# Optimization experiments

Measured on AMD Instinct MI355X. Metric: run time of the kernel, lower is better.

The kernel has to match this reference:

```python
import jax, jax.numpy as jnp
import numpy as np

NUM_CLASSES = 4
SIGMA_S = 1.0
SIGMA_Z = 1.0


def _rbf_gram(x, sigma):
    # x: [N, d] -> [N, N] Gaussian kernel exp(-||xi-xj||^2 / (2 sigma^2))
    sq = jnp.sum(x * x, axis=-1)
    d2 = sq[:, None] + sq[None, :] - 2.0 * (x @ x.T)
    d2 = jnp.maximum(d2, 0.0)
    return jnp.exp(-d2 / (2.0 * sigma * sigma))


def _double_center(K):
    # Faithful to: K = mean_center(K, dim=0); K_m = mean_center(K.t(), dim=0)
    K = K - jnp.mean(K, axis=0, keepdims=True)
    K = K.T
    K = K - jnp.mean(K, axis=0, keepdims=True)
    return K


def setup_inputs() -> dict:
    key = jax.random.key(0)
    kz, ks = jax.random.split(key)
    z = jax.random.normal(kz, (8192, 128), dtype=jnp.float32)
    s = jax.random.randint(ks, (8192,), 0, NUM_CLASSES, dtype=jnp.int64)
    norm = jnp.float32(1.0)
    return {"z": z, "s": s, "norm": norm}


def reference(z, s, norm):
    n = z.shape[0]
    s_onehot = jax.nn.one_hot(s, NUM_CLASSES, dtype=z.dtype)  # format_onehot
    K_sm = _double_center(_rbf_gram(s_onehot, SIGMA_S))
    K_zm = _double_center(_rbf_gram(z, SIGMA_Z))
    # trace(K_zm.T @ K_sm) == sum(K_zm * K_sm): O(N^2) instead of O(N^3)
    dep = jnp.sum(K_zm * K_sm)
    dep = dep / (norm * (n * n))
    return dep
```

## Files before the change

### kernel.cpp

```cpp
#include <hip/hip_runtime.h>
#include <hip/hip_bf16.h>

typedef float f32x4 __attribute__((ext_vector_type(4)));

#define ZD      128
#define BT      128
#define D2_CUT  60.0f
#define D2_TRIG 70.0f

__device__ __forceinline__ void async_copy16(const unsigned char* g,
                                             unsigned char* l) {
    __builtin_amdgcn_global_load_lds(
        (const __attribute__((address_space(1))) unsigned int*)g,
        (__attribute__((address_space(3))) unsigned int*)l,
        16, 0, 0);
}

__global__ __launch_bounds__(256) void dep_prep(
    const float* __restrict__ z, const int* __restrict__ s,
    float* __restrict__ sq, float* __restrict__ sqmin,
    unsigned char* __restrict__ zb8, float* __restrict__ pvals,
    const float* __restrict__ norm, float* __restrict__ out, int N)
{
    __shared__ float part[32][33];
    const int tid  = threadIdx.x;
    const int wave = tid >> 6, lane = tid & 63;
    const int half = lane >> 5, c = lane & 31;
    const int r0   = blockIdx.x * 32;

    if (blockIdx.x == 0 && wave == 2) {
        int c0 = 0, c1 = 0, c2 = 0, c3 = 0;
        for (int it = lane; it < N / 4; it += 64) {
            int4 v = ((const int4*)s)[it];
            c0 += (v.x == 0) + (v.y == 0) + (v.z == 0) + (v.w == 0);
            c1 += (v.x == 1) + (v.y == 1) + (v.z == 1) + (v.w == 1);
            c2 += (v.x == 2) + (v.y == 2) + (v.z == 2) + (v.w == 2);
            c3 += (v.x == 3) + (v.y == 3) + (v.z == 3) + (v.w == 3);
        }
        #pragma unroll
        for (int off = 1; off < 64; off <<= 1) {
            c0 += __shfl_xor(c0, off, 64);
            c1 += __shfl_xor(c1, off, 64);
            c2 += __shfl_xor(c2, off, 64);
            c3 += __shfl_xor(c3, off, 64);
        }
        if (lane == 0) {
            const double n = (double)N;
            const double p0 = c0 / n, p1 = c1 / n, p2 = c2 / n, p3 = c3 / n;
            const double sump2 = p0*p0 + p1*p1 + p2*p2 + p3*p3;
            const double scale = (1.0 - exp(-1.0)) / ((double)norm[0] * n * n);
            pvals[0] = (float)p0; pvals[1] = (float)p1;
            pvals[2] = (float)p2; pvals[3] = (float)p3;
            pvals[4] = (float)sump2;
            pvals[5] = (float)scale;
            const double c2sum = (double)c0*c0 + (double)c1*c1
                               + (double)c2*c2 + (double)c3*c3;
            const double diag = n - c2sum / n;
            out[0] = (float)(diag * scale);
        }
    }

    #pragma unroll
    for (int i = 0; i < 4; ++i) {
        const int rloc = wave * 8 + i * 2 + half;
        const int r    = r0 + rloc;
        float4 v = ((const float4*)z)[r * 32 + c];
        int pk = __builtin_amdgcn_cvt_pk_fp8_f32(v.x, v.y, 0, false);
        pk     = __builtin_amdgcn_cvt_pk_fp8_f32(v.z, v.w, pk, true);
        ((unsigned int*)zb8)[r * 32 + c] = (unsigned int)pk;
        part[rloc][c] = v.x*v.x + v.y*v.y + v.z*v.z + v.w*v.w;
    }
    __syncthreads();

    if (wave == 0 && lane < 32) {
        float sum = 0.f;
        #pragma unroll
        for (int k = 0; k < 32; ++k) sum += part[lane][k];
        sq[r0 + lane] = sum;
        float mn = sum;
        #pragma unroll
        for (int off = 1; off < 32; off <<= 1)
            mn = fminf(mn, __shfl_xor(mn, off, 64));
        if (lane == 0) sqmin[blockIdx.x] = mn;
    }
}

__global__ __launch_bounds__(256, 4) void dep_pair(
    const unsigned char* __restrict__ zb8, const float* __restrict__ sq,
    const float* __restrict__ sqmin, const int* __restrict__ s,
    const float* __restrict__ pvals, float* __restrict__ out, int T)
{
    __shared__ unsigned char Apan[BT * ZD];
    __shared__ unsigned char Bpan[BT * ZD];

    const int tid  = threadIdx.x;
    const int wave = tid >> 6, lane = tid & 63;

    const int t = blockIdx.x;
    #define TRI_BASE(x) ((x) * T - ((x) * ((x) - 1)) / 2)
    double disc = (2.0 * T + 1.0) * (2.0 * T + 1.0) - 8.0 * (double)t;
    int ti = (int)((2.0 * T + 1.0 - sqrt(disc)) * 0.5);
    if (ti < 0) ti = 0;
    if (ti > T - 1) ti = T - 1;
    while (ti + 1 < T && TRI_BASE(ti + 1) <= t) ++ti;
    while (ti > 0 && TRI_BASE(ti) > t) --ti;
    const int tj = ti + (t - TRI_BASE(ti));
    #undef TRI_BASE

    const int i0 = ti * BT, j0 = tj * BT;
    const int wi = wave >> 1, wj = wave & 1;
    const int l15 = lane & 15, quad = lane >> 4;

    {
        const unsigned char* gAp = zb8 + (size_t)i0 * ZD;
        const unsigned char* gBp = zb8 + (size_t)j0 * ZD;
        const int rl  = lane >> 3;
        const int cch = lane & 7;
        const int gch = cch ^ rl;
        #pragma unroll
        for (int k = 0; k < 4; ++k) {
            const int r0i = (wave * 4 + k) * 8;
            const size_t go = (size_t)(r0i + rl) * ZD + (gch << 4);
            async_copy16(gAp + go, Apan + r0i * ZD);
            async_copy16(gBp + go, Bpan + r0i * ZD);
        }
    }
    __syncthreads();

    f32x4 accv[4][4];
    #pragma unroll
    for (int a = 0; a < 4; ++a)
        #pragma unroll
        for (int b = 0; b < 4; ++b)
            accv[a][b] = (f32x4){0.f, 0.f, 0.f, 0.f};

    const int sub = (quad & 1) * 8;
    #pragma unroll
    for (int kc = 0; kc < 4; ++kc) {
        long af[4], bfr[4];
        const int ch = (kc * 2 + (quad >> 1)) ^ (l15 & 7);
        #pragma unroll
        for (int it = 0; it < 4; ++it) {
            const int row = wi * 64 + it * 16 + l15;
            af[it] = *(const long*)(Apan + row * ZD + (ch << 4) + sub);
        }
        #pragma unroll
        for (int jt = 0; jt < 4; ++jt) {
            const int row = wj * 64 + jt * 16 + l15;
            bfr[jt] = *(const long*)(Bpan + row * ZD + (ch << 4) + sub);
        }
        #pragma unroll
        for (int it = 0; it < 4; ++it)
            #pragma unroll
            for (int jt = 0; jt < 4; ++jt)
                accv[it][jt] = __builtin_amdgcn_mfma_f32_16x16x32_fp8_fp8(
                    af[it], bfr[jt], accv[it][jt], 0, 0, 0);
    }

    float m = -1e30f;
    #pragma unroll
    for (int it = 0; it < 4; ++it)
        #pragma unroll
        for (int jt = 0; jt < 4; ++jt) {
            const f32x4 v = accv[it][jt];
            m = fmaxf(m, fmaxf(fmaxf(v[0], v[1]), fmaxf(v[2], v[3])));
        }
    #pragma unroll
    for (int off = 1; off < 64; off <<= 1)
        m = fmaxf(m, __shfl_xor(m, off, 64));

    const int gA = (i0 >> 5) + wi * 2;
    const int gB = (j0 >> 5) + wj * 2;
    const float sminA = fminf(sqmin[gA], sqmin[gA + 1]);
    const float sminB = fminf(sqmin[gB], sqmin[gB + 1]);
    const float bound = sminA + sminB - 2.0f * m;

    if (bound < D2_TRIG) {
        const float p0 = pvals[0], p1 = pvals[1],
                    p2 = pvals[2], p3 = pvals[3];
        const float sump2 = pvals[4], scale = pvals[5];
        const float p[4] = {p0, p1, p2, p3};

        const int ibase = i0 + wi * 64, jbase = j0 + wj * 64;
        float sqj[4];
        #pragma unroll
        for (int jt = 0; jt < 4; ++jt) sqj[jt] = sq[jbase + jt * 16 + l15];

        float local = 0.f;
        #pragma unroll
        for (int it = 0; it < 4; ++it) {
            #pragma unroll
            for (int r = 0; r < 4; ++r) {
                const int i = ibase + it * 16 + quad * 4 + r;
                const float sqi = sq[i];
                #pragma unroll
                for (int jt = 0; jt < 4; ++jt) {
                    const int j = jbase + jt * 16 + l15;
                    float d2 = sqi + sqj[jt] - 2.0f * accv[it][jt][r];
                    d2 = fmaxf(d2, 0.0f);
                    if (d2 < D2_CUT && i != j) {
                        const int si = s[i], sj = s[j];
                        const float w = (si == sj ? 1.0f : 0.0f)
                                      - p[si] - p[sj] + sump2;
                        local += w * __expf(-0.5f * d2);
                    }
                }
            }
        }
        if (ti < tj) local *= 2.0f;

        #pragma unroll
        for (int off = 32; off > 0; off >>= 1)
            local += __shfl_down(local, off, 64);
        if (lane == 0 && local != 0.0f)
            atomicAdd(out, local * scale);
    }
}

extern "C" void kernel_launch(void* const* d_in, const int* in_sizes, int n_in,
                              void* d_out, int out_size, void* d_ws, size_t ws_size,
                              hipStream_t stream)
{
    const float* z    = (const float*)d_in[0];
    const int*   s    = (const int*)d_in[1];
    const float* norm = (const float*)d_in[2];
    float* out = (float*)d_out;

    const int N = in_sizes[1];
    const int T = N / BT;

    char* ws = (char*)d_ws;
    float*         pvals = (float*)ws;
    float*         sq    = (float*)(ws + 64);
    float*         sqmin = (float*)(ws + 64 + (size_t)N * 4);
    unsigned char* zb8   = (unsigned char*)(ws + 64 + (size_t)N * 4
                                            + (size_t)(N / 32) * 4);

    dep_prep<<<N / 32, 256, 0, stream>>>(z, s, sq, sqmin, zb8, pvals,
                                         norm, out, N);
    const int nblocks = T * (T + 1) / 2;
    dep_pair<<<nblocks, 256, 0, stream>>>(zb8, sq, sqmin, s, pvals, out, T);
}
```

Baseline: 77.91 us.

## Make pair kernel persistent with double-buffered LDS prefetch and tile map

The pair kernel becomes a persistent grid of 512 blocks that loops over triangular tile pairs, prefetching the next tile's A/B panels into a second LDS buffer while the current tile is computed. The per-block sqrt-based triangular index decode is replaced by a lookup table that the prep kernel writes. The aim is to hide global-to-LDS load latency and cut launch and decode overhead. In exchange LDS use doubles and the occupancy hint drops to 2 blocks per CU, so there is less parallelism across waves.

```diff
diff --git a/kernel.cpp b/kernel.cpp
--- a/kernel.cpp
+++ b/kernel.cpp
@@ -20,13 +20,21 @@
     const float* __restrict__ z, const int* __restrict__ s,
     float* __restrict__ sq, float* __restrict__ sqmin,
     unsigned char* __restrict__ zb8, float* __restrict__ pvals,
-    const float* __restrict__ norm, float* __restrict__ out, int N)
+    int* __restrict__ tmap, const float* __restrict__ norm,
+    float* __restrict__ out, int N, int T)
 {
     __shared__ float part[32][33];
     const int tid  = threadIdx.x;
     const int wave = tid >> 6, lane = tid & 63;
     const int half = lane >> 5, c = lane & 31;
     const int r0   = blockIdx.x * 32;
+
+    if (blockIdx.x == 0 && wave == 1 && lane < T) {
+        const int ti   = lane;
+        const int base = ti * T - (ti * (ti - 1)) / 2;
+        for (int tj = ti; tj < T; ++tj)
+            tmap[base + (tj - ti)] = (ti << 8) | tj;
+    }
 
     if (blockIdx.x == 0 && wave == 2) {
         int c0 = 0, c1 = 0, c2 = 0, c3 = 0;
@@ -85,135 +93,150 @@
     }
 }
 
-__global__ __launch_bounds__(256, 4) void dep_pair(
+__global__ __launch_bounds__(256, 2) void dep_pair(
     const unsigned char* __restrict__ zb8, const float* __restrict__ sq,
     const float* __restrict__ sqmin, const int* __restrict__ s,
-    const float* __restrict__ pvals, float* __restrict__ out, int T)
+    const float* __restrict__ pvals, const int* __restrict__ tmap,
+    float* __restrict__ out, int NT)
 {
-    __shared__ unsigned char Apan[BT * ZD];
-    __shared__ unsigned char Bpan[BT * ZD];
+    __shared__ unsigned char pan[2][2][BT * ZD];
 
     const int tid  = threadIdx.x;
     const int wave = tid >> 6, lane = tid & 63;
-
-    const int t = blockIdx.x;
-    #define TRI_BASE(x) ((x) * T - ((x) * ((x) - 1)) / 2)
-    double disc = (2.0 * T + 1.0) * (2.0 * T + 1.0) - 8.0 * (double)t;
-    int ti = (int)((2.0 * T + 1.0 - sqrt(disc)) * 0.5);
-    if (ti < 0) ti = 0;
-    if (ti > T - 1) ti = T - 1;
-    while (ti + 1 < T && TRI_BASE(ti + 1) <= t) ++ti;
-    while (ti > 0 && TRI_BASE(ti) > t) --ti;
-    const int tj = ti + (t - TRI_BASE(ti));
-    #undef TRI_BASE
-
-    const int i0 = ti * BT, j0 = tj * BT;
-    const int wi = wave >> 1, wj = wave & 1;
-    const int l15 = lane & 15, quad = lane >> 4;
-
-    {
-        const unsigned char* gAp = zb8 + (size_t)i0 * ZD;
-        const unsigned char* gBp = zb8 + (size_t)j0 * ZD;
-        const int rl  = lane >> 3;
-        const int cch = lane & 7;
-        const int gch = cch ^ rl;
+    const int wi   = wave >> 1, wj = wave & 1;
+    const int l15  = lane & 15, quad = lane >> 4;
+    const int rl   = lane >> 3, cch = lane & 7;
+    const int gch  = cch ^ rl;
+
+    int t = blockIdx.x;
+    if (t >= NT) return;
+
+    int mt = tmap[t];
+    int ti = mt >> 8, tj = mt & 255;
+
+    auto stage = [&](int sti, int stj, int buf) {
+        const unsigned char* gA = zb8 + (size_t)sti * BT * ZD;
+        const unsigned char* gB = zb8 + (size_t)stj * BT * ZD;
         #pragma unroll
         for (int k = 0; k < 4; ++k) {
             const int r0i = (wave * 4 + k) * 8;
             const size_t go = (size_t)(r0i + rl) * ZD + (gch << 4);
-            async_copy16(gAp + go, Apan + r0i * ZD);
-            async_copy16(gBp + go, Bpan + r0i * ZD);
-        }
-    }
+            async_copy16(gA + go, &pan[buf][0][r0i * ZD]);
+            async_copy16(gB + go, &pan[buf][1][r0i * ZD]);
+        }
+    };
+
+    stage(ti, tj, 0);
     __syncthreads();
-
-    f32x4 accv[4][4];
-    #pragma unroll
-    for (int a = 0; a < 4; ++a)
-        #pragma unroll
-        for (int b = 0; b < 4; ++b)
-            accv[a][b] = (f32x4){0.f, 0.f, 0.f, 0.f};
-
-    const int sub = (quad & 1) * 8;
-    #pragma unroll
-    for (int kc = 0; kc < 4; ++kc) {
-        long af[4], bfr[4];
-        const int ch = (kc * 2 + (quad >> 1)) ^ (l15 & 7);
-        #pragma unroll
-        for (int it = 0; it < 4; ++it) {
-            const int row = wi * 64 + it * 16 + l15;
-            af[it] = *(const long*)(Apan + row * ZD + (ch << 4) + sub);
-        }
-        #pragma unroll
-        for (int jt = 0; jt < 4; ++jt) {
-            const int row = wj * 64 + jt * 16 + l15;
-            bfr[jt] = *(const long*)(Bpan + row * ZD + (ch << 4) + sub);
-        }
+    int p = 0;
+
+    while (true) {
+        const int tn = t + gridDim.x;
+        const bool have = (tn < NT);
+        int nti = 0, ntj = 0;
+        if (have) {
+            const int m2 = tmap[tn];
+            nti = m2 >> 8; ntj = m2 & 255;
+            stage(nti, ntj, p ^ 1);
+        }
+
+        const int i0 = ti * BT, j0 = tj * BT;
+        const unsigned char* Apan = &pan[p][0][0];
+        const unsigned char* Bpan = &pan[p][1][0];
+
+        f32x4 accv[4][4];
+        #pragma unroll
+        for (int a = 0; a < 4; ++a)
+            #pragma unroll
+            for (int b = 0; b < 4; ++b)
+                accv[a][b] = (f32x4){0.f, 0.f, 0.f, 0.f};
+
+        const int sub = (quad & 1) * 8;
+        #pragma unroll
+        for (int kc = 0; kc < 4; ++kc) {
+            long af[4], bfr[4];
+            const int ch = (kc * 2 + (quad >> 1)) ^ (l15 & 7);
+            #pragma unroll
+            for (int it = 0; it < 4; ++it) {
+                const int row = wi * 64 + it * 16 + l15;
+                af[it] = *(const long*)(Apan + row * ZD + (ch << 4) + sub);
+            }
+            #pragma unroll
+            for (int jt = 0; jt < 4; ++jt) {
+                const int row = wj * 64 + jt * 16 + l15;
+                bfr[jt] = *(const long*)(Bpan + row * ZD + (ch << 4) + sub);
+            }
+            #pragma unroll
+            for (int it = 0; it < 4; ++it)
+                #pragma unroll
+                for (int jt = 0; jt < 4; ++jt)
+                    accv[it][jt] = __builtin_amdgcn_mfma_f32_16x16x32_fp8_fp8(
+                        af[it], bfr[jt], accv[it][jt], 0, 0, 0);
+        }
+
+        float m = -1e30f;
         #pragma unroll
         for (int it = 0; it < 4; ++it)
             #pragma unroll
+            for (int jt = 0; jt < 4; ++jt) {
+                const f32x4 v = accv[it][jt];
+                m = fmaxf(m, fmaxf(fmaxf(v[0], v[1]), fmaxf(v[2], v[3])));
+            }
+        #pragma unroll
+        for (int off = 1; off < 64; off <<= 1)
+            m = fmaxf(m, __shfl_xor(m, off, 64));
+
+        const int gA = (i0 >> 5) + wi * 2;
+        const int gB = (j0 >> 5) + wj * 2;
+        const float sminA = fminf(sqmin[gA], sqmin[gA + 1]);
+        const float sminB = fminf(sqmin[gB], sqmin[gB + 1]);
+        const float bound = sminA + sminB - 2.0f * m;
+
+        if (bound < D2_TRIG) {
+            const float p0 = pvals[0], p1 = pvals[1],
+                        p2 = pvals[2], p3 = pvals[3];
+            const float sump2 = pvals[4], scale = pvals[5];
+            const float pr[4] = {p0, p1, p2, p3};
+
+            const int ibase = i0 + wi * 64, jbase = j0 + wj * 64;
+            float sqj[4];
+            #pragma unroll
             for (int jt = 0; jt < 4; ++jt)
-                accv[it][jt] = __builtin_amdgcn_mfma_f32_16x16x32_fp8_fp8(
-                    af[it], bfr[jt], accv[it][jt], 0, 0, 0);
-    }
-
-    float m = -1e30f;
-    #pragma unroll
-    for (int it = 0; it < 4; ++it)
-        #pragma unroll
-        for (int jt = 0; jt < 4; ++jt) {
-            const f32x4 v = accv[it][jt];
-            m = fmaxf(m, fmaxf(fmaxf(v[0], v[1]), fmaxf(v[2], v[3])));
-        }
-    #pragma unroll
-    for (int off = 1; off < 64; off <<= 1)
-        m = fmaxf(m, __shfl_xor(m, off, 64));
-
-    const int gA = (i0 >> 5) + wi * 2;
-    const int gB = (j0 >> 5) + wj * 2;
-    const float sminA = fminf(sqmin[gA], sqmin[gA + 1]);
-    const float sminB = fminf(sqmin[gB], sqmin[gB + 1]);
-    const float bound = sminA + sminB - 2.0f * m;
-
-    if (bound < D2_TRIG) {
-        const float p0 = pvals[0], p1 = pvals[1],
-                    p2 = pvals[2], p3 = pvals[3];
-        const float sump2 = pvals[4], scale = pvals[5];
-        const float p[4] = {p0, p1, p2, p3};
-
-        const int ibase = i0 + wi * 64, jbase = j0 + wj * 64;
-        float sqj[4];
-        #pragma unroll
-        for (int jt = 0; jt < 4; ++jt) sqj[jt] = sq[jbase + jt * 16 + l15];
-
-        float local = 0.f;
-        #pragma unroll
-        for (int it = 0; it < 4; ++it) {
-            #pragma unroll
-            for (int r = 0; r < 4; ++r) {
-                const int i = ibase + it * 16 + quad * 4 + r;
-                const float sqi = sq[i];
+                sqj[jt] = sq[jbase + jt * 16 + l15];
+
+            float local = 0.f;
+            #pragma unroll
+            for (int it = 0; it < 4; ++it) {
                 #pragma unroll
-                for (int jt = 0; jt < 4; ++jt) {
-                    const int j = jbase + jt * 16 + l15;
-                    float d2 = sqi + sqj[jt] - 2.0f * accv[it][jt][r];
-                    d2 = fmaxf(d2, 0.0f);
-                    if (d2 < D2_CUT && i != j) {
-                        const int si = s[i], sj = s[j];
-                        const float w = (si == sj ? 1.0f : 0.0f)
-                                      - p[si] - p[sj] + sump2;
-                        local += w * __expf(-0.5f * d2);
+                for (int r = 0; r < 4; ++r) {
+                    const int i = ibase + it * 16 + quad * 4 + r;
+                    const float sqi = sq[i];
+                    #pragma unroll
+                    for (int jt = 0; jt < 4; ++jt) {
+                        const int j = jbase + jt * 16 + l15;
+                        float d2 = sqi + sqj[jt] - 2.0f * accv[it][jt][r];
+                        d2 = fmaxf(d2, 0.0f);
+                        if (d2 < D2_CUT && i != j) {
+                            const int si = s[i], sj = s[j];
+                            const float w = (si == sj ? 1.0f : 0.0f)
+                                          - pr[si] - pr[sj] + sump2;
+                            local += w * __expf(-0.5f * d2);
+                        }
                     }
                 }
             }
-        }
-        if (ti < tj) local *= 2.0f;
-
-        #pragma unroll
-        for (int off = 32; off > 0; off >>= 1)
-            local += __shfl_down(local, off, 64);
-        if (lane == 0 && local != 0.0f)
-            atomicAdd(out, local * scale);
+            if (ti < tj) local *= 2.0f;
+
+            #pragma unroll
+            for (int off = 32; off > 0; off >>= 1)
+                local += __shfl_down(local, off, 64);
+            if (lane == 0 && local != 0.0f)
+                atomicAdd(out, local * scale);
+        }
+
+        __syncthreads();
+        if (!have) break;
+        t = tn; ti = nti; tj = ntj; p ^= 1;
     }
 }
 
@@ -226,18 +249,22 @@
     const float* norm = (const float*)d_in[2];
     float* out = (float*)d_out;
 
-    const int N = in_sizes[1];
-    const int T = N / BT;
+    const int N  = in_sizes[1];
+    const int T  = N / BT;
+    const int NT = T * (T + 1) / 2;
 
     char* ws = (char*)d_ws;
     float*         pvals = (float*)ws;
     float*         sq    = (float*)(ws + 64);
     float*         sqmin = (float*)(ws + 64 + (size_t)N * 4);
+    int*           tmap  = (int*)(ws + 64 + (size_t)N * 4
+                                  + (size_t)(N / 32) * 4);
     unsigned char* zb8   = (unsigned char*)(ws + 64 + (size_t)N * 4
-                                            + (size_t)(N / 32) * 4);
-
-    dep_prep<<<N / 32, 256, 0, stream>>>(z, s, sq, sqmin, zb8, pvals,
-                                         norm, out, N);
-    const int nblocks = T * (T + 1) / 2;
-    dep_pair<<<nblocks, 256, 0, stream>>>(zb8, sq, sqmin, s, pvals, out, T);
-}
+                                  + (size_t)(N / 32) * 4
+                                  + (((size_t)NT * 4 + 63) & ~63ull));
+
+    dep_prep<<<N / 32, 256, 0, stream>>>(z, s, sq, sqmin, zb8, pvals, tmap,
+                                         norm, out, N, T);
+    dep_pair<<<512, 256, 0, stream>>>(zb8, sq, sqmin, s, pvals, tmap,
+                                      out, NT);
+}
```

Result: slower. 80.97 us (+3.9%).
